# Kernel optimization log

Hardware: AMD Instinct MI355X
Metric: run time of the kernel (lower is better)

The kernel has to match this reference:

```python
import jax, jax.numpy as jnp
import numpy as np


def gatv2(x, src, dst, ea, Wl, bl, Wr, br, We, att, bias, N):
    # PyG GATv2Conv: source/target projections, edge embedding, leaky_relu(0.2)
    # attention, segment softmax over incoming edges, scatter-add aggregation.
    H, C = att.shape
    xl = (x @ Wl.T + bl).reshape(-1, H, C)   # [N,H,C] (source / message features)
    xr = (x @ Wr.T + br).reshape(-1, H, C)   # [N,H,C] (target features)
    ee = (ea @ We.T).reshape(-1, H, C)       # [E,H,C] edge embedding
    e = jax.nn.leaky_relu(xl[src] + xr[dst] + ee, 0.2)   # [E,H,C]
    s = jnp.einsum('ehc,hc->eh', e, att)                  # [E,H] scores
    smax = jax.ops.segment_max(s, dst, num_segments=N)
    ex = jnp.exp(s - smax[dst])
    den = jax.ops.segment_sum(ex, dst, num_segments=N)
    a = ex / (den[dst] + 1e-16)                           # segment softmax
    out = jax.ops.segment_sum(a[:, :, None] * xl[src], dst, num_segments=N)
    return out.reshape(N, H * C) + bias


def _forward(x, edge_index, edge_attr, actions, Wl1, bl1, Wr1, br1, We1, att1, bias1,
             Wl2, bl2, Wr2, br2, We2, att2, bias2, Wf, bf, Wp, bp, alpha):
    N = x.shape[0]
    E = edge_attr.shape[0]
    num_actions = E + 1
    src, dst = edge_index[0], edge_index[1]
    # add_self_loops(fill_value='mean'): self-loop edge_attr = per-node mean of incoming edge_attr
    cnt = jax.ops.segment_sum(jnp.ones((E,), x.dtype), dst, num_segments=N)
    mean_ea = jax.ops.segment_sum(edge_attr, dst, num_segments=N) / jnp.maximum(cnt, 1.0)[:, None]
    loop = jnp.arange(N, dtype=src.dtype)
    src2 = jnp.concatenate([src, loop])
    dst2 = jnp.concatenate([dst, loop])
    ea2 = jnp.concatenate([edge_attr, mean_ea], axis=0)
    h = jax.nn.relu(gatv2(x, src2, dst2, ea2, Wl1, bl1, Wr1, br1, We1, att1, bias1, N))
    h = jax.nn.relu(gatv2(h, src2, dst2, ea2, Wl2, bl2, Wr2, br2, We2, att2, bias2, N))
    g = jnp.mean(h, axis=0, keepdims=True)              # global_mean_pool, single graph -> [1,hid]
    state_potential = jax.nn.relu(g @ Wp.T + bp)[:, 0]  # [1]
    diag = jnp.concatenate([src != dst, jnp.array([True])])  # [E+1]
    logits = (g @ Wf.T + bf)[:, :num_actions]           # [1, E+1]
    amask = jnp.ones((num_actions,), bool).at[actions].set(False)
    mask = amask & diag
    logits = jnp.where(mask[None, :], logits, -jnp.inf)
    return jax.nn.softmax(logits, axis=1), state_potential, jax.nn.sigmoid(alpha)


def setup_inputs() -> dict:
    key = jax.random.key(0)
    ks = jax.random.split(key, 16)
    N, E, F, hid, H, A = 20000, 400000, 128, 64, 4, 450000
    x = jax.random.normal(ks[0], (N, F), jnp.float32)
    src = jax.random.randint(ks[1], (E,), 0, N)
    dst = (src + 1 + jax.random.randint(ks[2], (E,), 0, N - 1)) % N  # no pre-existing self loops
    edge_index = jnp.stack([src, dst])
    edge_attr = jax.random.normal(ks[3], (E, 1), jnp.float32)
    actions = jax.random.randint(ks[4], (128,), 0, E + 1)
    s = 0.05
    nrm = lambda k, shp: jax.random.normal(k, shp, jnp.float32) * s
    return {
        'x': x, 'edge_index': edge_index, 'edge_attr': edge_attr, 'actions': actions,
        'Wl1': nrm(ks[5], (H * hid, F)), 'bl1': jnp.zeros(H * hid),
        'Wr1': nrm(ks[6], (H * hid, F)), 'br1': jnp.zeros(H * hid),
        'We1': nrm(ks[7], (H * hid, 1)), 'att1': nrm(ks[8], (H, hid)), 'bias1': jnp.zeros(H * hid),
        'Wl2': nrm(ks[9], (hid, H * hid)), 'bl2': jnp.zeros(hid),
        'Wr2': nrm(ks[10], (hid, H * hid)), 'br2': jnp.zeros(hid),
        'We2': nrm(ks[11], (hid, 1)), 'att2': nrm(ks[12], (1, hid)), 'bias2': jnp.zeros(hid),
        'Wf': nrm(ks[13], (A, hid)), 'bf': jnp.zeros(A),
        'Wp': nrm(ks[14], (1, hid)), 'bp': jnp.zeros(1),
        'alpha': jnp.asarray(0.0, jnp.float32),
    }


def reference(x, edge_index, edge_attr, actions, Wl1, bl1, Wr1, br1, We1, att1, bias1,
              Wl2, bl2, Wr2, br2, We2, att2, bias2, Wf, bf, Wp, bp, alpha):
    return _forward(x, edge_index, edge_attr, actions, Wl1, bl1, Wr1, br1, We1, att1, bias1,
                    Wl2, bl2, Wr2, br2, We2, att2, bias2, Wf, bf, Wp, bp, alpha)
```

## Files before the change

kernel.cpp:

```cpp
#include <hip/hip_runtime.h>
#include <math.h>

typedef __attribute__((ext_vector_type(8))) short short8;
typedef __attribute__((ext_vector_type(4))) float f32x4;
typedef __attribute__((ext_vector_type(2))) float f32x2;

__device__ __forceinline__ float wred_sum(float v) {
#pragma unroll
  for (int off = 32; off; off >>= 1) v += __shfl_xor(v, off, 64);
  return v;
}
__device__ __forceinline__ float b2f(unsigned short u) {
  return __uint_as_float(((unsigned)u) << 16);
}
__device__ __forceinline__ unsigned short f2b(float f) {
  unsigned b = __float_as_uint(f);
  return (unsigned short)((b + 0x7FFFu + ((b >> 16) & 1u)) >> 16);
}
__device__ __forceinline__ unsigned char f2fp8(float v) {
  int pk = __builtin_amdgcn_cvt_pk_fp8_f32(v, v, 0, false);
  return (unsigned char)(pk & 0xFF);
}

__global__ __launch_bounds__(256) void k_prep(
    const float* __restrict__ s0, ushort* __restrict__ d0, int n0,
    const float* __restrict__ s1, ushort* __restrict__ d1, int n1,
    const float* __restrict__ s2, ushort* __restrict__ d2, int n2,
    const float* __restrict__ s3, ushort* __restrict__ d3, int n3,
    const float* __restrict__ s4, ushort* __restrict__ d4, int n4,
    const int* __restrict__ dstv, const float* __restrict__ ea,
    int* __restrict__ cnt_i, float* __restrict__ sum_ea,
    int* __restrict__ rank, int E,
    const int* __restrict__ actions, unsigned char* __restrict__ aflag,
    int n_act, int castB) {
  int b = blockIdx.x, tid = threadIdx.x;
  if (b == 0 && tid < n_act) aflag[actions[tid]] = 1;
  if (b < castB) {
    int t = (b * 256 + tid) * 4;
    const float* s; ushort* d; int off = t;
    if (off < n0) { s = s0; d = d0; }
    else { off -= n0;
      if (off < n1) { s = s1; d = d1; }
      else { off -= n1;
        if (off < n2) { s = s2; d = d2; }
        else { off -= n2;
          if (off < n3) { s = s3; d = d3; }
          else { off -= n3;
            if (off < n4) { s = s4; d = d4; }
            else return; } } } }
    float4 v = *(const float4*)(s + off);
    ushort4 o;
    o.x = f2b(v.x); o.y = f2b(v.y); o.z = f2b(v.z); o.w = f2b(v.w);
    *(ushort4*)(d + off) = o;
    return;
  }
  int e = (b - castB) * 256 + tid;
  if (e >= E) return;
  int d = dstv[e];
  int r = atomicAdd(&cnt_i[d], 1);
  atomicAdd(&sum_ea[d], ea[e]);
  __builtin_nontemporal_store(r, &rank[e]);
}

__global__ __launch_bounds__(1024) void k_scan(const int* __restrict__ cnt_i,
    int* __restrict__ row_st, int N) {
  __shared__ int ws[16];
  int tid = threadIdx.x;
  int lane = tid & 63, w = tid >> 6;
  int running = 0;
  for (int base = 0; base < N; base += 1024) {
    int i = base + tid;
    int c = (i < N) ? (cnt_i[i] + 1) : 0;
    int inc = c;
#pragma unroll
    for (int off = 1; off < 64; off <<= 1) {
      int u = __shfl_up(inc, off, 64);
      if (lane >= off) inc += u;
    }
    if (lane == 63) ws[w] = inc;
    __syncthreads();
    if (tid < 16) {
      int s = ws[tid];
#pragma unroll
      for (int off = 1; off < 16; off <<= 1) {
        int u = __shfl_up(s, off, 16);
        if (tid >= off) s += u;
      }
      ws[tid] = s;
    }
    __syncthreads();
    int woff = (w == 0) ? 0 : ws[w - 1];
    int total = ws[15];
    int ex = running + woff + (inc - c);
    if (i < N) row_st[i] = ex;
    running += total;
    __syncthreads();
  }
  if (tid == 0) row_st[N] = running;
}

__global__ __launch_bounds__(256) void k_gemm_scatter(const ushort* __restrict__ A,
    const ushort* __restrict__ W0, const float* __restrict__ b0,
    unsigned char* __restrict__ C0fp8,
    const ushort* __restrict__ W1, const float* __restrict__ b1,
    ushort* __restrict__ C1,
    int M, int Nc, int K,
    const int* __restrict__ dstv, const int* __restrict__ srcv,
    const float* __restrict__ ea, const int* __restrict__ cnt_i,
    const float* __restrict__ sum_ea, const int* __restrict__ rank,
    const int* __restrict__ row_st, unsigned* __restrict__ epack,
    int E, int E2) {
  int tid = threadIdx.x;
  if (blockIdx.z == 2) {
    int flat = blockIdx.x * gridDim.y + blockIdx.y;
    int stride = gridDim.x * gridDim.y * 256;
    for (int e = flat * 256 + tid; e < E2; e += stride) {
      int d, sn, rk; float av;
      if (e < E) { d = dstv[e]; sn = srcv[e]; av = ea[e]; rk = rank[e]; }
      else {
        d = e - E; sn = d;
        int c = cnt_i[d];
        av = sum_ea[d] / fmaxf((float)c, 1.0f);
        rk = c;
      }
      int pos = row_st[d] + rk;
      epack[pos] = ((unsigned)f2b(av) << 16) | (unsigned)sn;
    }
    return;
  }
  const ushort* W = blockIdx.z ? W1 : W0;
  const float* bias = blockIdx.z ? b1 : b0;
  int wave = tid >> 6, lane = tid & 63;
  int m0 = blockIdx.x * 64 + wave * 16;
  int n0 = blockIdx.y * 64;
  int r = lane & 15, g = lane >> 4;
  f32x4 acc[4] = {};
  int am = min(m0 + r, M - 1);
  const ushort* Arow = A + (size_t)am * K + g * 8;
  const ushort* Wrow = W + (size_t)(n0 + r) * K + g * 8;
  for (int k0 = 0; k0 < K; k0 += 32) {
    short8 a = *(const short8*)(const void*)(Arow + k0);
#pragma unroll
    for (int c = 0; c < 4; ++c) {
      short8 b = *(const short8*)(const void*)(Wrow + (size_t)c * 16 * K + k0);
      acc[c] = __builtin_amdgcn_mfma_f32_16x16x32_bf16(a, b, acc[c], 0, 0, 0);
    }
  }
#pragma unroll
  for (int c = 0; c < 4; ++c) {
    int gn = n0 + c * 16 + r;
    float bv = bias[gn];
#pragma unroll
    for (int j = 0; j < 4; ++j) {
      int gm = m0 + g * 4 + j;
      if (gm < M) {
        float v = acc[c][j] + bv;
        if (blockIdx.z == 0) C0fp8[(size_t)gm * Nc + gn] = f2fp8(v);
        else                 C1[(size_t)gm * Nc + gn] = f2b(v);
      }
    }
  }
}

__global__ __launch_bounds__(256) void k_gemm_mfma2(const ushort* __restrict__ A,
    const ushort* __restrict__ W0, const float* __restrict__ b0,
    unsigned char* __restrict__ C0fp8,
    const ushort* __restrict__ W1, const float* __restrict__ b1,
    ushort* __restrict__ C1,
    int M, int Nc, int K) {
  const ushort* W = blockIdx.z ? W1 : W0;
  const float* bias = blockIdx.z ? b1 : b0;
  int wave = threadIdx.x >> 6, lane = threadIdx.x & 63;
  int m0 = blockIdx.x * 64 + wave * 16;
  int n0 = blockIdx.y * 64;
  int r = lane & 15, g = lane >> 4;
  f32x4 acc[4] = {};
  int am = min(m0 + r, M - 1);
  const ushort* Arow = A + (size_t)am * K + g * 8;
  const ushort* Wrow = W + (size_t)(n0 + r) * K + g * 8;
  for (int k0 = 0; k0 < K; k0 += 32) {
    short8 a = *(const short8*)(const void*)(Arow + k0);
#pragma unroll
    for (int c = 0; c < 4; ++c) {
      short8 b = *(const short8*)(const void*)(Wrow + (size_t)c * 16 * K + k0);
      acc[c] = __builtin_amdgcn_mfma_f32_16x16x32_bf16(a, b, acc[c], 0, 0, 0);
    }
  }
#pragma unroll
  for (int c = 0; c < 4; ++c) {
    int gn = n0 + c * 16 + r;
    float bv = bias[gn];
#pragma unroll
    for (int j = 0; j < 4; ++j) {
      int gm = m0 + g * 4 + j;
      if (gm < M) {
        float v = acc[c][j] + bv;
        if (blockIdx.z == 0) C0fp8[(size_t)gm * Nc + gn] = f2fp8(v);
        else                 C1[(size_t)gm * Nc + gn] = f2b(v);
      }
    }
  }
}

__global__ __launch_bounds__(256) void k_fused1(const unsigned char* __restrict__ xl8,
    const ushort* __restrict__ xr, const unsigned* __restrict__ epack,
    const int* __restrict__ row_st,
    const float* __restrict__ We, const float* __restrict__ att,
    const float* __restrict__ bias, ushort* __restrict__ out, int N) {
  int tid = threadIdx.x;
  int lane = tid & 63;
  int half = lane >> 5, l32 = lane & 31;
  int n = blockIdx.x * 8 + (tid >> 6) * 2 + half;
  if (n >= N) return;
  int c0 = l32 * 8;
  float4 Wa = *(const float4*)(We + c0), Wb = *(const float4*)(We + c0 + 4);
  float4 Aa = *(const float4*)(att + c0), Ab = *(const float4*)(att + c0 + 4);
  float Wev[8] = {Wa.x, Wa.y, Wa.z, Wa.w, Wb.x, Wb.y, Wb.z, Wb.w};
  float atv[8] = {Aa.x, Aa.y, Aa.z, Aa.w, Ab.x, Ab.y, Ab.z, Ab.w};
  short8 xru = *(const short8*)(const void*)(xr + (size_t)n * 256 + c0);
  float xrf[8];
#pragma unroll
  for (int j = 0; j < 8; ++j) xrf[j] = b2f((unsigned short)xru[j]);
  int a = row_st[n], b = row_st[n + 1];
  float m = -INFINITY, den = 0.f;
  float acc[8] = {};
  int i = a;
  for (; i + 1 < b; i += 2) {
    unsigned p0 = epack[i], p1 = epack[i + 1];
    int sn0 = (int)(p0 & 0xFFFFu), sn1 = (int)(p1 & 0xFFFFu);
    float av0 = b2f((unsigned short)(p0 >> 16));
    float av1 = b2f((unsigned short)(p1 >> 16));
    uint2 u0 = *(const uint2*)(const void*)(xl8 + (size_t)sn0 * 256 + c0);
    uint2 u1 = *(const uint2*)(const void*)(xl8 + (size_t)sn1 * 256 + c0);
    float x0[8], x1[8];
    {
      f32x2 da = __builtin_amdgcn_cvt_pk_f32_fp8(u0.x, false);
      f32x2 db = __builtin_amdgcn_cvt_pk_f32_fp8(u0.x, true);
      f32x2 dc = __builtin_amdgcn_cvt_pk_f32_fp8(u0.y, false);
      f32x2 dd = __builtin_amdgcn_cvt_pk_f32_fp8(u0.y, true);
      x0[0] = da[0]; x0[1] = da[1]; x0[2] = db[0]; x0[3] = db[1];
      x0[4] = dc[0]; x0[5] = dc[1]; x0[6] = dd[0]; x0[7] = dd[1];
      da = __builtin_amdgcn_cvt_pk_f32_fp8(u1.x, false);
      db = __builtin_amdgcn_cvt_pk_f32_fp8(u1.x, true);
      dc = __builtin_amdgcn_cvt_pk_f32_fp8(u1.y, false);
      dd = __builtin_amdgcn_cvt_pk_f32_fp8(u1.y, true);
      x1[0] = da[0]; x1[1] = da[1]; x1[2] = db[0]; x1[3] = db[1];
      x1[4] = dc[0]; x1[5] = dc[1]; x1[6] = dd[0]; x1[7] = dd[1];
    }
    float t0 = 0.f, t1 = 0.f;
#pragma unroll
    for (int j = 0; j < 8; ++j) {
      float v0 = x0[j] + xrf[j] + av0 * Wev[j];
      float v1 = x1[j] + xrf[j] + av1 * Wev[j];
      v0 = v0 > 0.f ? v0 : 0.2f * v0;
      v1 = v1 > 0.f ? v1 : 0.2f * v1;
      t0 += atv[j] * v0;
      t1 += atv[j] * v1;
    }
    t0 += __shfl_xor(t0, 1, 8); t1 += __shfl_xor(t1, 1, 8);
    t0 += __shfl_xor(t0, 2, 8); t1 += __shfl_xor(t1, 2, 8);
    t0 += __shfl_xor(t0, 4, 8); t1 += __shfl_xor(t1, 4, 8);
    float tm = fmaxf(t0, t1);
    if (tm > m) {
      float sc = __expf(m - tm);
      m = tm; den *= sc;
#pragma unroll
      for (int j = 0; j < 8; ++j) acc[j] *= sc;
    }
    float e0 = __expf(t0 - m), e1 = __expf(t1 - m);
    den += e0 + e1;
#pragma unroll
    for (int j = 0; j < 8; ++j) acc[j] += e0 * x0[j] + e1 * x1[j];
  }
  if (i < b) {
    unsigned pr = epack[i];
    int sn = (int)(pr & 0xFFFFu);
    float av = b2f((unsigned short)(pr >> 16));
    uint2 u = *(const uint2*)(const void*)(xl8 + (size_t)sn * 256 + c0);
    float x[8];
    f32x2 da = __builtin_amdgcn_cvt_pk_f32_fp8(u.x, false);
    f32x2 db = __builtin_amdgcn_cvt_pk_f32_fp8(u.x, true);
    f32x2 dc = __builtin_amdgcn_cvt_pk_f32_fp8(u.y, false);
    f32x2 dd = __builtin_amdgcn_cvt_pk_f32_fp8(u.y, true);
    x[0] = da[0]; x[1] = da[1]; x[2] = db[0]; x[3] = db[1];
    x[4] = dc[0]; x[5] = dc[1]; x[6] = dd[0]; x[7] = dd[1];
    float t = 0.f;
#pragma unroll
    for (int j = 0; j < 8; ++j) {
      float v = x[j] + xrf[j] + av * Wev[j];
      v = v > 0.f ? v : 0.2f * v;
      t += atv[j] * v;
    }
    t += __shfl_xor(t, 1, 8);
    t += __shfl_xor(t, 2, 8);
    t += __shfl_xor(t, 4, 8);
    if (t > m) {
      float sc = __expf(m - t);
      m = t; den *= sc;
#pragma unroll
      for (int j = 0; j < 8; ++j) acc[j] *= sc;
    }
    float ex = __expf(t - m);
    den += ex;
#pragma unroll
    for (int j = 0; j < 8; ++j) acc[j] += ex * x[j];
  }
  float inv = 1.f / (den + 1e-16f);
  float4 Ba = *(const float4*)(bias + c0), Bb = *(const float4*)(bias + c0 + 4);
  float bv[8] = {Ba.x, Ba.y, Ba.z, Ba.w, Bb.x, Bb.y, Bb.z, Bb.w};
  short8 o;
#pragma unroll
  for (int j = 0; j < 8; ++j) o[j] = (short)f2b(fmaxf(acc[j] * inv + bv[j], 0.f));
  *(short8*)(void*)(out + (size_t)n * 256 + c0) = o;
}

__global__ __launch_bounds__(256) void k_fused2(const unsigned char* __restrict__ xl8,
    const ushort* __restrict__ xr, const unsigned* __restrict__ epack,
    const int* __restrict__ row_st,
    const float* __restrict__ We, const float* __restrict__ att,
    const float* __restrict__ bias, float* __restrict__ g_sum, int N) {
  __shared__ float gred[4][64];
  int tid = threadIdx.x;
  int lane = tid & 63, w = tid >> 6;
  int sub = lane >> 3, l8 = lane & 7;
  int n = blockIdx.x * 32 + w * 8 + sub;
  bool valid = n < N;
  int c0 = l8 * 8;
  float4 Wa = *(const float4*)(We + c0), Wb = *(const float4*)(We + c0 + 4);
  float4 Aa = *(const float4*)(att + c0), Ab = *(const float4*)(att + c0 + 4);
  float Wev[8] = {Wa.x, Wa.y, Wa.z, Wa.w, Wb.x, Wb.y, Wb.z, Wb.w};
  float atv[8] = {Aa.x, Aa.y, Aa.z, Aa.w, Ab.x, Ab.y, Ab.z, Ab.w};
  float xrf[8] = {};
  if (valid) {
    short8 xru = *(const short8*)(const void*)(xr + (size_t)n * 64 + c0);
#pragma unroll
    for (int j = 0; j < 8; ++j) xrf[j] = b2f((unsigned short)xru[j]);
  }
  int a = 0, b = 0;
  if (valid) { a = row_st[n]; b = row_st[n + 1]; }
  float m = -INFINITY, den = 0.f;
  float acc[8] = {};
  int i = a;
  for (; i + 1 < b; i += 2) {
    unsigned p0 = epack[i], p1 = epack[i + 1];
    int sn0 = (int)(p0 & 0xFFFFu), sn1 = (int)(p1 & 0xFFFFu);
    float av0 = b2f((unsigned short)(p0 >> 16));
    float av1 = b2f((unsigned short)(p1 >> 16));
    uint2 u0 = *(const uint2*)(const void*)(xl8 + (size_t)sn0 * 64 + c0);
    uint2 u1 = *(const uint2*)(const void*)(xl8 + (size_t)sn1 * 64 + c0);
    float x0[8], x1[8];
    {
      f32x2 da = __builtin_amdgcn_cvt_pk_f32_fp8(u0.x, false);
      f32x2 db = __builtin_amdgcn_cvt_pk_f32_fp8(u0.x, true);
      f32x2 dc = __builtin_amdgcn_cvt_pk_f32_fp8(u0.y, false);
      f32x2 dd = __builtin_amdgcn_cvt_pk_f32_fp8(u0.y, true);
      x0[0] = da[0]; x0[1] = da[1]; x0[2] = db[0]; x0[3] = db[1];
      x0[4] = dc[0]; x0[5] = dc[1]; x0[6] = dd[0]; x0[7] = dd[1];
      da = __builtin_amdgcn_cvt_pk_f32_fp8(u1.x, false);
      db = __builtin_amdgcn_cvt_pk_f32_fp8(u1.x, true);
      dc = __builtin_amdgcn_cvt_pk_f32_fp8(u1.y, false);
      dd = __builtin_amdgcn_cvt_pk_f32_fp8(u1.y, true);
      x1[0] = da[0]; x1[1] = da[1]; x1[2] = db[0]; x1[3] = db[1];
      x1[4] = dc[0]; x1[5] = dc[1]; x1[6] = dd[0]; x1[7] = dd[1];
    }
    float t0 = 0.f, t1 = 0.f;
#pragma unroll
    for (int j = 0; j < 8; ++j) {
      float v0 = x0[j] + xrf[j] + av0 * Wev[j];
      float v1 = x1[j] + xrf[j] + av1 * Wev[j];
      v0 = v0 > 0.f ? v0 : 0.2f * v0;
      v1 = v1 > 0.f ? v1 : 0.2f * v1;
      t0 += atv[j] * v0;
      t1 += atv[j] * v1;
    }
    t0 += __shfl_xor(t0, 1, 8); t1 += __shfl_xor(t1, 1, 8);
    t0 += __shfl_xor(t0, 2, 8); t1 += __shfl_xor(t1, 2, 8);
    t0 += __shfl_xor(t0, 4, 8); t1 += __shfl_xor(t1, 4, 8);
    float tm = fmaxf(t0, t1);
    if (tm > m) {
      float sc = __expf(m - tm);
      m = tm; den *= sc;
#pragma unroll
      for (int j = 0; j < 8; ++j) acc[j] *= sc;
    }
    float e0 = __expf(t0 - m), e1 = __expf(t1 - m);
    den += e0 + e1;
#pragma unroll
    for (int j = 0; j < 8; ++j) acc[j] += e0 * x0[j] + e1 * x1[j];
  }
  if (i < b) {
    unsigned pr = epack[i];
    int sn = (int)(pr & 0xFFFFu);
    float av = b2f((unsigned short)(pr >> 16));
    uint2 u = *(const uint2*)(const void*)(xl8 + (size_t)sn * 64 + c0);
    float x[8];
    f32x2 da = __builtin_amdgcn_cvt_pk_f32_fp8(u.x, false);
    f32x2 db = __builtin_amdgcn_cvt_pk_f32_fp8(u.x, true);
    f32x2 dc = __builtin_amdgcn_cvt_pk_f32_fp8(u.y, false);
    f32x2 dd = __builtin_amdgcn_cvt_pk_f32_fp8(u.y, true);
    x[0] = da[0]; x[1] = da[1]; x[2] = db[0]; x[3] = db[1];
    x[4] = dc[0]; x[5] = dc[1]; x[6] = dd[0]; x[7] = dd[1];
    float t = 0.f;
#pragma unroll
    for (int j = 0; j < 8; ++j) {
      float v = x[j] + xrf[j] + av * Wev[j];
      v = v > 0.f ? v : 0.2f * v;
      t += atv[j] * v;
    }
    t += __shfl_xor(t, 1, 8);
    t += __shfl_xor(t, 2, 8);
    t += __shfl_xor(t, 4, 8);
    if (t > m) {
      float sc = __expf(m - t);
      m = t; den *= sc;
#pragma unroll
      for (int j = 0; j < 8; ++j) acc[j] *= sc;
    }
    float ex = __expf(t - m);
    den += ex;
#pragma unroll
    for (int j = 0; j < 8; ++j) acc[j] += ex * x[j];
  }
  float inv = 1.f / (den + 1e-16f);
  float4 Ba = *(const float4*)(bias + c0), Bb = *(const float4*)(bias + c0 + 4);
  float bv[8] = {Ba.x, Ba.y, Ba.z, Ba.w, Bb.x, Bb.y, Bb.z, Bb.w};
  float vals[8];
#pragma unroll
  for (int j = 0; j < 8; ++j)
    vals[j] = valid ? fmaxf(acc[j] * inv + bv[j], 0.f) : 0.f;
#pragma unroll
  for (int j = 0; j < 8; ++j) {
    float v = vals[j];
    v += __shfl_xor(v, 8, 64);
    v += __shfl_xor(v, 16, 64);
    v += __shfl_xor(v, 32, 64);
    vals[j] = v;
  }
  if (lane < 8) {
#pragma unroll
    for (int j = 0; j < 8; ++j) gred[w][lane * 8 + j] = vals[j];
  }
  __syncthreads();
  if (tid < 64)
    atomicAdd(&g_sum[tid], gred[0][tid] + gred[1][tid] + gred[2][tid] + gred[3][tid]);
}

__global__ __launch_bounds__(256) void k_logits(const float* __restrict__ g_sum,
    const float* __restrict__ Wp, const float* __restrict__ bp,
    const float* __restrict__ alpha,
    const float* __restrict__ Wf, const float* __restrict__ bf,
    const unsigned char* __restrict__ aflag, const int* __restrict__ src,
    const int* __restrict__ dst, float* __restrict__ exps,
    float* __restrict__ gsum, float* __restrict__ out,
    int E, int NA, float invN) {
  __shared__ float gs[64];
  __shared__ float wsum[4];
  int tid = threadIdx.x;
  if (tid < 64) gs[tid] = g_sum[tid] * invN;
  __syncthreads();
  if (blockIdx.x == 0 && tid < 64) {
    float t = wred_sum(gs[tid] * Wp[tid]);
    if (tid == 0) {
      float sp = t + bp[0];
      out[NA] = sp > 0.f ? sp : 0.f;
      out[NA + 1] = 1.f / (1.f + __expf(-alpha[0]));
    }
  }
  int j0 = tid & 3;
  int row0 = blockIdx.x * 128 + (tid >> 2);
  int row1 = row0 + 64;
  float gv[4];
  {
    const float4* g4 = (const float4*)gs;
#pragma unroll
    for (int u = 0; u < 4; ++u) {
      float4 t4 = g4[j0 + u * 4];
      gv[u * 1] = 0;
    }
  }
  const float4* g4 = (const float4*)gs;
  float4 gva = g4[j0], gvb = g4[j0 + 4], gvc = g4[j0 + 8], gvd = g4[j0 + 12];
  float ex0 = 0.f, ex1 = 0.f;
  bool r0ok = row0 < NA, r1ok = row1 < NA;
  float acc0 = 0.f, acc1 = 0.f;
  if (r0ok) {
    const float4* wr = (const float4*)(Wf + (size_t)row0 * 64);
    float4 w0 = wr[j0], w1 = wr[j0 + 4], w2 = wr[j0 + 8], w3 = wr[j0 + 12];
    acc0 = w0.x * gva.x + w0.y * gva.y + w0.z * gva.z + w0.w * gva.w
         + w1.x * gvb.x + w1.y * gvb.y + w1.z * gvb.z + w1.w * gvb.w
         + w2.x * gvc.x + w2.y * gvc.y + w2.z * gvc.z + w2.w * gvc.w
         + w3.x * gvd.x + w3.y * gvd.y + w3.z * gvd.z + w3.w * gvd.w;
  }
  if (r1ok) {
    const float4* wr = (const float4*)(Wf + (size_t)row1 * 64);
    float4 w0 = wr[j0], w1 = wr[j0 + 4], w2 = wr[j0 + 8], w3 = wr[j0 + 12];
    acc1 = w0.x * gva.x + w0.y * gva.y + w0.z * gva.z + w0.w * gva.w
         + w1.x * gvb.x + w1.y * gvb.y + w1.z * gvb.z + w1.w * gvb.w
         + w2.x * gvc.x + w2.y * gvc.y + w2.z * gvc.z + w2.w * gvc.w
         + w3.x * gvd.x + w3.y * gvd.y + w3.z * gvd.z + w3.w * gvd.w;
  }
  acc0 += __shfl_xor(acc0, 1, 4); acc1 += __shfl_xor(acc1, 1, 4);
  acc0 += __shfl_xor(acc0, 2, 4); acc1 += __shfl_xor(acc1, 2, 4);
  if (j0 == 0) {
    if (r0ok) {
      bool keep = (!aflag[row0]) && (row0 >= E || src[row0] != dst[row0]);
      ex0 = keep ? __expf(acc0 + bf[row0]) : 0.f;
      exps[row0] = ex0;
    }
    if (r1ok) {
      bool keep = (!aflag[row1]) && (row1 >= E || src[row1] != dst[row1]);
      ex1 = keep ? __expf(acc1 + bf[row1]) : 0.f;
      exps[row1] = ex1;
    }
  }
  float s = wred_sum(ex0 + ex1);
  if ((tid & 63) == 0) wsum[tid >> 6] = s;
  __syncthreads();
  if (tid == 0)
    atomicAdd(&gsum[blockIdx.x & 63],
              wsum[0] + wsum[1] + wsum[2] + wsum[3]);
}

__global__ __launch_bounds__(256) void k_norm(const float* __restrict__ exps,
    const float* __restrict__ gsum, float* __restrict__ out, int NA) {
  int tid = threadIdx.x;
  float total = gsum[tid & 63];
  total = wred_sum(total);
  float inv = 1.f / total;
  int i = (blockIdx.x * 256 + tid) * 4;
  if (i >= NA) return;
  if (i + 3 < NA) {
    float4 v = *(const float4*)(exps + i);
    float4 o;
    o.x = v.x * inv; o.y = v.y * inv; o.z = v.z * inv; o.w = v.w * inv;
    *(float4*)(out + i) = o;
  } else {
    for (int j = i; j < NA; ++j) out[j] = exps[j] * inv;
  }
}

extern "C" void kernel_launch(void* const* d_in, const int* in_sizes, int n_in,
                              void* d_out, int out_size, void* d_ws, size_t ws_size,
                              hipStream_t stream) {
  const float* x      = (const float*)d_in[0];
  const int*   eidx   = (const int*)d_in[1];
  const float* eattr  = (const float*)d_in[2];
  const int*   actions= (const int*)d_in[3];
  const float* Wl1 = (const float*)d_in[4];
  const float* bl1 = (const float*)d_in[5];
  const float* Wr1 = (const float*)d_in[6];
  const float* br1 = (const float*)d_in[7];
  const float* We1 = (const float*)d_in[8];
  const float* att1= (const float*)d_in[9];
  const float* bias1=(const float*)d_in[10];
  const float* Wl2 = (const float*)d_in[11];
  const float* bl2 = (const float*)d_in[12];
  const float* Wr2 = (const float*)d_in[13];
  const float* br2 = (const float*)d_in[14];
  const float* We2 = (const float*)d_in[15];
  const float* att2= (const float*)d_in[16];
  const float* bias2=(const float*)d_in[17];
  const float* Wf  = (const float*)d_in[18];
  const float* bf  = (const float*)d_in[19];
  const float* Wp  = (const float*)d_in[20];
  const float* bp  = (const float*)d_in[21];
  const float* alpha=(const float*)d_in[22];

  const int F = 128;
  const int N = in_sizes[0] / F;
  const int E = in_sizes[2];
  const int E2 = E + N;
  const int NA = E + 1;
  const int n_act = in_sizes[3];
  const int* src = eidx;
  const int* dst = eidx + E;

  float* ws = (float*)d_ws;
  size_t p = 0;
  int*      cnt_i    = (int*)(ws + p);      p += (size_t)N;
  float*    sum_ea   = ws + p;              p += (size_t)N;
  float*    g_sum    = ws + p;              p += 64;
  float*    gsum     = ws + p;              p += 64;
  unsigned char* aflag = (unsigned char*)(ws + p); p += ((size_t)NA + 3) / 4;
  size_t zero_bytes = p * sizeof(float);
  int*      row_st   = (int*)(ws + p);      p += (size_t)N + 64;
  int*      rank     = (int*)(ws + p);      p += (size_t)E;
  unsigned* epack    = (unsigned*)(ws + p); p += (size_t)E2;
  float*    exps     = ws + p;              p += (size_t)NA + 64;
  unsigned char* xl8 = (unsigned char*)(ws + p); p += (size_t)N * 256 / 4;
  unsigned char* xl28 = (unsigned char*)(ws + p); p += (size_t)N * 64 / 4;
  ushort* ub = (ushort*)(ws + p);
  size_t q = 0;
  ushort* xb   = ub + q; q += (size_t)N * F;
  ushort* wl1b = ub + q; q += (size_t)256 * 128;
  ushort* wr1b = ub + q; q += (size_t)256 * 128;
  ushort* wl2b = ub + q; q += (size_t)64 * 256;
  ushort* wr2b = ub + q; q += (size_t)64 * 256;
  ushort* xr1b = ub + q; q += (size_t)N * 256;
  ushort* h1b  = ub + q; q += (size_t)N * 256;
  ushort* xr2b = ub + q; q += (size_t)N * 64;

  float* out = (float*)d_out;

  hipMemsetAsync(d_ws, 0, zero_bytes, stream);

  {
    int n0 = N * F, n1 = 256 * 128, n2 = 256 * 128, n3 = 64 * 256, n4 = 64 * 256;
    int tot4 = (n0 + n1 + n2 + n3 + n4) / 4;
    int castB = (tot4 + 255) / 256;
    int cntB = (E + 255) / 256;
    k_prep<<<castB + cntB, 256, 0, stream>>>(
        x, xb, n0, Wl1, wl1b, n1, Wr1, wr1b, n2, Wl2, wl2b, n3, Wr2, wr2b, n4,
        dst, eattr, cnt_i, sum_ea, rank, E, actions, aflag, n_act, castB);
  }

  k_scan<<<1, 1024, 0, stream>>>(cnt_i, row_st, N);

  {
    dim3 g1((N + 63) / 64, 4, 3);
    k_gemm_scatter<<<g1, 256, 0, stream>>>(xb, wl1b, bl1, xl8, wr1b, br1, xr1b,
                                           N, 256, 128,
                                           dst, src, eattr, cnt_i, sum_ea,
                                           rank, row_st, epack, E, E2);
  }
  k_fused1<<<(N + 7) / 8, 256, 0, stream>>>(xl8, xr1b, epack, row_st,
                                            We1, att1, bias1, h1b, N);
  {
    dim3 g2((N + 63) / 64, 1, 2);
    k_gemm_mfma2<<<g2, 256, 0, stream>>>(h1b, wl2b, bl2, xl28, wr2b, br2, xr2b,
                                         N, 64, 256);
  }
  k_fused2<<<(N + 31) / 32, 256, 0, stream>>>(xl28, xr2b, epack, row_st,
                                              We2, att2, bias2, g_sum, N);

  k_logits<<<(NA + 127) / 128, 256, 0, stream>>>(
      g_sum, Wp, bp, alpha, Wf, bf, aflag, src, dst,
      exps, gsum, out, E, NA, 1.0f / (float)N);
  int nb4 = (NA + 1023) / 1024;
  k_norm<<<nb4, 256, 0, stream>>>(exps, gsum, out, NA);
}
```

Baseline: 243.7 us.

## Fuse row-offset scan into prep kernel via last-block-done counter

Removes the separate single-block scan launch by having the last block to finish k_prep, detected with an atomic done counter and threadfences, perform the exclusive scan of per-node counts. The scan now runs on 256 threads instead of 1024, so it takes more serial iterations over N. Action flags switch from a byte array to a bitmask built with atomicOr, which also shrinks the memset region. Dead code in k_logits is removed.

```diff
diff --git a/kernel.cpp b/kernel.cpp
--- a/kernel.cpp
+++ b/kernel.cpp
@@ -31,13 +31,19 @@
     const int* __restrict__ dstv, const float* __restrict__ ea,
     int* __restrict__ cnt_i, float* __restrict__ sum_ea,
     int* __restrict__ rank, int E,
-    const int* __restrict__ actions, unsigned char* __restrict__ aflag,
-    int n_act, int castB) {
+    const int* __restrict__ actions, unsigned* __restrict__ abits,
+    int n_act, int castB,
+    int* __restrict__ done_ctr, int* __restrict__ row_st, int N) {
+  __shared__ int wtot[4];
+  __shared__ int lastFlag;
   int b = blockIdx.x, tid = threadIdx.x;
-  if (b == 0 && tid < n_act) aflag[actions[tid]] = 1;
+  if (b == 0 && tid < n_act) {
+    int a = actions[tid];
+    atomicOr(&abits[a >> 5], 1u << (a & 31));
+  }
   if (b < castB) {
     int t = (b * 256 + tid) * 4;
-    const float* s; ushort* d; int off = t;
+    const float* s = 0; ushort* d = 0; int off = t;
     if (off < n0) { s = s0; d = d0; }
     else { off -= n0;
       if (off < n1) { s = s1; d = d1; }
@@ -46,57 +52,56 @@
         else { off -= n2;
           if (off < n3) { s = s3; d = d3; }
           else { off -= n3;
-            if (off < n4) { s = s4; d = d4; }
-            else return; } } } }
-    float4 v = *(const float4*)(s + off);
-    ushort4 o;
-    o.x = f2b(v.x); o.y = f2b(v.y); o.z = f2b(v.z); o.w = f2b(v.w);
-    *(ushort4*)(d + off) = o;
-    return;
-  }
-  int e = (b - castB) * 256 + tid;
-  if (e >= E) return;
-  int d = dstv[e];
-  int r = atomicAdd(&cnt_i[d], 1);
-  atomicAdd(&sum_ea[d], ea[e]);
-  __builtin_nontemporal_store(r, &rank[e]);
-}
-
-__global__ __launch_bounds__(1024) void k_scan(const int* __restrict__ cnt_i,
-    int* __restrict__ row_st, int N) {
-  __shared__ int ws[16];
-  int tid = threadIdx.x;
-  int lane = tid & 63, w = tid >> 6;
-  int running = 0;
-  for (int base = 0; base < N; base += 1024) {
-    int i = base + tid;
-    int c = (i < N) ? (cnt_i[i] + 1) : 0;
-    int inc = c;
-#pragma unroll
-    for (int off = 1; off < 64; off <<= 1) {
-      int u = __shfl_up(inc, off, 64);
-      if (lane >= off) inc += u;
-    }
-    if (lane == 63) ws[w] = inc;
-    __syncthreads();
-    if (tid < 16) {
-      int s = ws[tid];
-#pragma unroll
-      for (int off = 1; off < 16; off <<= 1) {
-        int u = __shfl_up(s, off, 16);
-        if (tid >= off) s += u;
+            if (off < n4) { s = s4; d = d4; } } } } }
+    if (s) {
+      float4 v = *(const float4*)(s + off);
+      ushort4 o;
+      o.x = f2b(v.x); o.y = f2b(v.y); o.z = f2b(v.z); o.w = f2b(v.w);
+      *(ushort4*)(d + off) = o;
+    }
+  } else {
+    int e = (b - castB) * 256 + tid;
+    if (e < E) {
+      int d = dstv[e];
+      int r = atomicAdd(&cnt_i[d], 1);
+      atomicAdd(&sum_ea[d], ea[e]);
+      __builtin_nontemporal_store(r, &rank[e]);
+    }
+  }
+  __syncthreads();
+  if (tid == 0) {
+    __threadfence();
+    int old = atomicAdd(done_ctr, 1);
+    lastFlag = (old == (int)gridDim.x - 1);
+  }
+  __syncthreads();
+  if (lastFlag) {
+    __threadfence();
+    int lane = tid & 63, w = tid >> 6;
+    int running = 0;
+    for (int base = 0; base < N; base += 256) {
+      int i = base + tid;
+      int c = (i < N) ? (cnt_i[i] + 1) : 0;
+      int inc = c;
+#pragma unroll
+      for (int off2 = 1; off2 < 64; off2 <<= 1) {
+        int u = __shfl_up(inc, off2, 64);
+        if (lane >= off2) inc += u;
       }
-      ws[tid] = s;
-    }
-    __syncthreads();
-    int woff = (w == 0) ? 0 : ws[w - 1];
-    int total = ws[15];
-    int ex = running + woff + (inc - c);
-    if (i < N) row_st[i] = ex;
-    running += total;
-    __syncthreads();
-  }
-  if (tid == 0) row_st[N] = running;
+      if (lane == 63) wtot[w] = inc;
+      __syncthreads();
+      int woff = 0;
+#pragma unroll
+      for (int k = 0; k < 4; ++k)
+        if (k < w) woff += wtot[k];
+      int total = wtot[0] + wtot[1] + wtot[2] + wtot[3];
+      int ex = running + woff + inc - c;
+      if (i < N) row_st[i] = ex;
+      running += total;
+      __syncthreads();
+    }
+    if (tid == 0) row_st[N] = running;
+  }
 }
 
 __global__ __launch_bounds__(256) void k_gemm_scatter(const ushort* __restrict__ A,
@@ -449,7 +454,7 @@
     const float* __restrict__ Wp, const float* __restrict__ bp,
     const float* __restrict__ alpha,
     const float* __restrict__ Wf, const float* __restrict__ bf,
-    const unsigned char* __restrict__ aflag, const int* __restrict__ src,
+    const unsigned* __restrict__ abits, const int* __restrict__ src,
     const int* __restrict__ dst, float* __restrict__ exps,
     float* __restrict__ gsum, float* __restrict__ out,
     int E, int NA, float invN) {
@@ -469,15 +474,6 @@
   int j0 = tid & 3;
   int row0 = blockIdx.x * 128 + (tid >> 2);
   int row1 = row0 + 64;
-  float gv[4];
-  {
-    const float4* g4 = (const float4*)gs;
-#pragma unroll
-    for (int u = 0; u < 4; ++u) {
-      float4 t4 = g4[j0 + u * 4];
-      gv[u * 1] = 0;
-    }
-  }
   const float4* g4 = (const float4*)gs;
   float4 gva = g4[j0], gvb = g4[j0 + 4], gvc = g4[j0 + 8], gvd = g4[j0 + 12];
   float ex0 = 0.f, ex1 = 0.f;
@@ -503,12 +499,14 @@
   acc0 += __shfl_xor(acc0, 2, 4); acc1 += __shfl_xor(acc1, 2, 4);
   if (j0 == 0) {
     if (r0ok) {
-      bool keep = (!aflag[row0]) && (row0 >= E || src[row0] != dst[row0]);
+      bool masked = (abits[row0 >> 5] >> (row0 & 31)) & 1u;
+      bool keep = (!masked) && (row0 >= E || src[row0] != dst[row0]);
       ex0 = keep ? __expf(acc0 + bf[row0]) : 0.f;
       exps[row0] = ex0;
     }
     if (r1ok) {
-      bool keep = (!aflag[row1]) && (row1 >= E || src[row1] != dst[row1]);
+      bool masked = (abits[row1 >> 5] >> (row1 & 31)) & 1u;
+      bool keep = (!masked) && (row1 >= E || src[row1] != dst[row1]);
       ex1 = keep ? __expf(acc1 + bf[row1]) : 0.f;
       exps[row1] = ex1;
     }
@@ -581,7 +579,8 @@
   float*    sum_ea   = ws + p;              p += (size_t)N;
   float*    g_sum    = ws + p;              p += 64;
   float*    gsum     = ws + p;              p += 64;
-  unsigned char* aflag = (unsigned char*)(ws + p); p += ((size_t)NA + 3) / 4;
+  int*      done_ctr = (int*)(ws + p);      p += 64;
+  unsigned* abits    = (unsigned*)(ws + p); p += ((size_t)NA + 31) / 32 + 16;
   size_t zero_bytes = p * sizeof(float);
   int*      row_st   = (int*)(ws + p);      p += (size_t)N + 64;
   int*      rank     = (int*)(ws + p);      p += (size_t)E;
@@ -611,10 +610,9 @@
     int cntB = (E + 255) / 256;
     k_prep<<<castB + cntB, 256, 0, stream>>>(
         x, xb, n0, Wl1, wl1b, n1, Wr1, wr1b, n2, Wl2, wl2b, n3, Wr2, wr2b, n4,
-        dst, eattr, cnt_i, sum_ea, rank, E, actions, aflag, n_act, castB);
-  }
-
-  k_scan<<<1, 1024, 0, stream>>>(cnt_i, row_st, N);
+        dst, eattr, cnt_i, sum_ea, rank, E, actions, abits, n_act, castB,
+        done_ctr, row_st, N);
+  }
 
   {
     dim3 g1((N + 63) / 64, 4, 3);
@@ -634,7 +632,7 @@
                                               We2, att2, bias2, g_sum, N);
 
   k_logits<<<(NA + 127) / 128, 256, 0, stream>>>(
-      g_sum, Wp, bp, alpha, Wf, bf, aflag, src, dst,
+      g_sum, Wp, bp, alpha, Wf, bf, abits, src, dst,
       exps, gsum, out, E, NA, 1.0f / (float)N);
   int nb4 = (NA + 1023) / 1024;
   k_norm<<<nb4, 256, 0, stream>>>(exps, gsum, out, NA);
```

Result: slower. 339.5 us (+39.3%).
